# Optimization experiments

Measured on AMD Instinct MI355X. Metric: run time of the kernel, lower is better.

Reference implementation:

```python
import jax, jax.numpy as jnp
import numpy as np

N_SRC = 2_000_000
N_TAR = 2_000_000

def _make_covs(key, n):
    # 3x3 SPD block embedded in a 4x4 (last row/col zero), as in GICP covariances
    A = jax.random.normal(key, (n, 3, 3), dtype=jnp.float32)
    cov3 = 0.1 * jnp.einsum('nij,nkj->nik', A, A) + 0.1 * jnp.eye(3, dtype=jnp.float32)
    covs = jnp.zeros((n, 4, 4), dtype=jnp.float32)
    return covs.at[:, :3, :3].set(cov3)

def setup_inputs() -> dict:
    key = jax.random.key(0)
    k1, k2, k3, k4, k5, k6 = jax.random.split(key, 6)
    # homogeneous points (x, y, z, 1)
    src_xyz = jax.random.normal(k1, (N_SRC, 3), dtype=jnp.float32) * 5.0
    tar_xyz = jax.random.normal(k2, (N_TAR, 3), dtype=jnp.float32) * 5.0
    ones_s = jnp.ones((N_SRC, 1), dtype=jnp.float32)
    ones_t = jnp.ones((N_TAR, 1), dtype=jnp.float32)
    src_points = jnp.concatenate([src_xyz, ones_s], axis=1)
    tar_points = jnp.concatenate([tar_xyz, ones_t], axis=1)
    covs_src = _make_covs(k3, N_SRC)
    covs_tar = _make_covs(k4, N_TAR)
    # transformation: near-identity SE(3)-ish 4x4 (param in the original model)
    transformation = jnp.eye(4, dtype=jnp.float32) + 0.01 * jax.random.normal(k5, (4, 4), dtype=jnp.float32)
    # nearest-neighbor indices (kdtree result in the original, non-differentiable)
    nearest_indices = jax.random.randint(k6, (N_SRC,), 0, N_TAR, dtype=jnp.int64 if jax.config.jax_enable_x64 else jnp.int32)
    return {
        'transformation': transformation,
        'src_points': src_points,
        'tar_points': tar_points,
        'covs_src': covs_src,
        'covs_tar': covs_tar,
        'nearest_indices': nearest_indices,
    }

def reference(transformation, src_points, tar_points, covs_src, covs_tar, nearest_indices):
    # transformed_src_points = src_points @ T  (N,4)
    transformed_src = src_points @ transformation
    # gather KNN-matched target points / covariances
    sel_tar = tar_points[nearest_indices]          # (N,4)
    sel_covs_tar = covs_tar[nearest_indices]       # (N,4,4)
    # T @ C_src @ T^T per point
    tcov = jnp.einsum('ij,njk,lk->nil', transformation, covs_src, transformation)
    RCR = sel_covs_tar + tcov                      # (N,4,4)
    inv_RCR = jnp.linalg.inv(RCR[:, :3, :3])       # (N,3,3)
    res = sel_tar[:, :3] - transformed_src[:, :3]  # (N,3)
    maha = jnp.einsum('ni,nij,nj->n', res, inv_RCR, res)
    return 0.5 * jnp.mean(maha)
```

## Files before the change

### kernel.cpp

```cpp
#include <hip/hip_runtime.h>
#include <stdint.h>

#define BLOCK        256
#define UNROLL       4
#define MAX_BLOCKS   4096

typedef float f32x4 __attribute__((ext_vector_type(4)));

__device__ __forceinline__ float gicp_point(
    int i,
    const float t00, const float t01, const float t02,
    const float t10, const float t11, const float t12,
    const float t20, const float t21, const float t22,
    const float t30, const float t31, const float t32,
    const f32x4* __restrict__ src, const f32x4* __restrict__ tar,
    const f32x4* __restrict__ cs,  const f32x4* __restrict__ ct,
    const int*   __restrict__ idx)
{
    const int   j  = __builtin_nontemporal_load(&idx[i]);
    const f32x4 s  = __builtin_nontemporal_load(&src[i]);
    const f32x4 tp = tar[j];

    const size_t bj = (size_t)j * 4;
    const f32x4 d0 = ct[bj + 0];
    const f32x4 d1 = ct[bj + 1];
    const f32x4 d2 = ct[bj + 2];

    const size_t bi = (size_t)i * 4;
    const f32x4 c0 = __builtin_nontemporal_load(&cs[bi + 0]);
    const f32x4 c1 = __builtin_nontemporal_load(&cs[bi + 1]);
    const f32x4 c2 = __builtin_nontemporal_load(&cs[bi + 2]);

    const float ts0 = s.x * t00 + s.y * t10 + s.z * t20 + s.w * t30;
    const float ts1 = s.x * t01 + s.y * t11 + s.z * t21 + s.w * t31;
    const float ts2 = s.x * t02 + s.y * t12 + s.z * t22 + s.w * t32;
    const float r0 = tp.x - ts0;
    const float r1 = tp.y - ts1;
    const float r2 = tp.z - ts2;

    const float u00 = t00*c0.x + t01*c1.x + t02*c2.x;
    const float u01 = t00*c0.y + t01*c1.y + t02*c2.y;
    const float u02 = t00*c0.z + t01*c1.z + t02*c2.z;
    const float u10 = t10*c0.x + t11*c1.x + t12*c2.x;
    const float u11 = t10*c0.y + t11*c1.y + t12*c2.y;
    const float u12 = t10*c0.z + t11*c1.z + t12*c2.z;
    const float u20 = t20*c0.x + t21*c1.x + t22*c2.x;
    const float u21 = t20*c0.y + t21*c1.y + t22*c2.y;
    const float u22 = t20*c0.z + t21*c1.z + t22*c2.z;

    const float tc00 = u00*t00 + u01*t01 + u02*t02;
    const float tc01 = u00*t10 + u01*t11 + u02*t12;
    const float tc02 = u00*t20 + u01*t21 + u02*t22;
    const float tc11 = u10*t10 + u11*t11 + u12*t12;
    const float tc12 = u10*t20 + u11*t21 + u12*t22;
    const float tc22 = u20*t20 + u21*t21 + u22*t22;

    const float a = d0.x + tc00;
    const float b = d0.y + tc01;
    const float c = d0.z + tc02;
    const float d = d1.y + tc11;
    const float e = d1.z + tc12;
    const float f = d2.z + tc22;

    const float A00 = d * f - e * e;
    const float A01 = c * e - b * f;
    const float A02 = b * e - c * d;
    const float A11 = a * f - c * c;
    const float A12 = b * c - a * e;
    const float A22 = a * d - b * b;

    const float det = a * A00 + b * A01 + c * A02;

    const float num = r0 * r0 * A00 + r1 * r1 * A11 + r2 * r2 * A22
                    + 2.0f * (r0 * r1 * A01 + r0 * r2 * A02 + r1 * r2 * A12);

    return num / det;
}

__global__ __launch_bounds__(BLOCK) void gicp_maha_kernel(
    const float* __restrict__ T,
    const f32x4* __restrict__ src,
    const f32x4* __restrict__ tar,
    const f32x4* __restrict__ cs,
    const f32x4* __restrict__ ct,
    const int*   __restrict__ idx,
    float*       __restrict__ partial,
    int n)
{
    const float t00 = T[0],  t01 = T[1],  t02 = T[2];
    const float t10 = T[4],  t11 = T[5],  t12 = T[6];
    const float t20 = T[8],  t21 = T[9],  t22 = T[10];
    const float t30 = T[12], t31 = T[13], t32 = T[14];

    const int stride = gridDim.x * BLOCK;
    const int step   = stride * UNROLL;

    float local = 0.0f;
    for (int base = blockIdx.x * BLOCK + threadIdx.x; base < n; base += step) {
        if (base + 3 * stride < n) {
            float v0 = gicp_point(base,            t00,t01,t02,t10,t11,t12,t20,t21,t22,t30,t31,t32, src,tar,cs,ct,idx);
            float v1 = gicp_point(base +   stride, t00,t01,t02,t10,t11,t12,t20,t21,t22,t30,t31,t32, src,tar,cs,ct,idx);
            float v2 = gicp_point(base + 2*stride, t00,t01,t02,t10,t11,t12,t20,t21,t22,t30,t31,t32, src,tar,cs,ct,idx);
            float v3 = gicp_point(base + 3*stride, t00,t01,t02,t10,t11,t12,t20,t21,t22,t30,t31,t32, src,tar,cs,ct,idx);
            local += (v0 + v1) + (v2 + v3);
        } else {
            #pragma unroll
            for (int k = 0; k < UNROLL; ++k) {
                int i = base + k * stride;
                const float m = (i < n) ? 1.0f : 0.0f;
                i = (i < n) ? i : (n - 1);
                local += m * gicp_point(i, t00,t01,t02,t10,t11,t12,t20,t21,t22,t30,t31,t32, src,tar,cs,ct,idx);
            }
        }
    }

    for (int off = 32; off > 0; off >>= 1)
        local += __shfl_down(local, off, 64);

    __shared__ float wsum[BLOCK / 64];
    const int wave = threadIdx.x >> 6;
    if ((threadIdx.x & 63) == 0) wsum[wave] = local;
    __syncthreads();
    if (threadIdx.x == 0) {
        float s = wsum[0];
        #pragma unroll
        for (int w = 1; w < BLOCK / 64; ++w) s += wsum[w];
        partial[blockIdx.x] = s;
    }
}

__global__ __launch_bounds__(256) void gicp_finalize_kernel(
    const float* __restrict__ partial, float* __restrict__ out,
    double scale, int nblocks)
{
    double s = 0.0;
    for (int k = threadIdx.x; k < nblocks; k += 256)
        s += (double)partial[k];
    for (int off = 32; off > 0; off >>= 1)
        s += __shfl_down(s, off, 64);
    __shared__ double wsum[4];
    const int wave = threadIdx.x >> 6;
    if ((threadIdx.x & 63) == 0) wsum[wave] = s;
    __syncthreads();
    if (threadIdx.x == 0)
        out[0] = (float)((wsum[0] + wsum[1] + wsum[2] + wsum[3]) * scale);
}

extern "C" void kernel_launch(void* const* d_in, const int* in_sizes, int n_in,
                              void* d_out, int out_size, void* d_ws, size_t ws_size,
                              hipStream_t stream) {
    const float* T   = (const float*)d_in[0];
    const f32x4* src = (const f32x4*)d_in[1];
    const f32x4* tar = (const f32x4*)d_in[2];
    const f32x4* cs  = (const f32x4*)d_in[3];
    const f32x4* ct  = (const f32x4*)d_in[4];
    const int*   idx = (const int*)d_in[5];
    const int n = in_sizes[1] / 4;

    int nblocks = (n + BLOCK * UNROLL - 1) / (BLOCK * UNROLL);
    if (nblocks < 1) nblocks = 1;
    if (nblocks > MAX_BLOCKS) nblocks = MAX_BLOCKS;
    const int ws_cap = (int)(ws_size / sizeof(float));
    if (nblocks > ws_cap) nblocks = ws_cap;

    float* partial = (float*)d_ws;

    gicp_maha_kernel<<<nblocks, BLOCK, 0, stream>>>(T, src, tar, cs, ct, idx,
                                                    partial, n);
    gicp_finalize_kernel<<<1, 256, 0, stream>>>(partial, (float*)d_out,
                                                0.5 / (double)n, nblocks);
}
```

Baseline: 351.6 us.

## Prepack target covariance and point into one 64-byte record for gathers

Adds a pre-pass that interleaves the first three target covariance rows with the target point into one 64-byte record per target. The main kernel's random gather then touches a single cache line per neighbour instead of two separate arrays. When the workspace is too small to hold the records, it instead runs a cache-warming pass that streams the target arrays before the direct kernel. The pre-pass adds a full extra read and write of the target data each call. The record buffer is sized from the source count rather than the target count.

```diff
diff --git a/kernel.cpp b/kernel.cpp
--- a/kernel.cpp
+++ b/kernel.cpp
@@ -1,36 +1,51 @@
 #include <hip/hip_runtime.h>
 #include <stdint.h>
 
-#define BLOCK        256
-#define UNROLL       4
-#define MAX_BLOCKS   4096
+#define BLOCK          256
+#define UNROLL         4
+#define MAX_BLOCKS     4096
+#define PREPACK_BLOCKS 2048
+#define WARM_BLOCKS    2048
 
 typedef float f32x4 __attribute__((ext_vector_type(4)));
 
-__device__ __forceinline__ float gicp_point(
-    int i,
+__global__ __launch_bounds__(256) void prepack_kernel(
+    const f32x4* __restrict__ tar,
+    const f32x4* __restrict__ ct,
+    f32x4*       __restrict__ rec,
+    long n4)
+{
+    const long stride = (long)gridDim.x * 256;
+    for (long k = (long)blockIdx.x * 256 + threadIdx.x; k < n4; k += stride) {
+        f32x4 v;
+        if ((k & 3) == 3) v = __builtin_nontemporal_load(&tar[k >> 2]);
+        else              v = __builtin_nontemporal_load(&ct[k]);
+        rec[k] = v;
+    }
+}
+
+__global__ __launch_bounds__(256) void llc_warm_kernel(
+    const f32x4* __restrict__ tar, long ntar4,
+    const f32x4* __restrict__ ct,  long nct4)
+{
+    const long stride = (long)gridDim.x * 256;
+    f32x4 acc = {0.f, 0.f, 0.f, 0.f};
+    for (long k = (long)blockIdx.x * 256 + threadIdx.x; k < nct4; k += stride)
+        acc += ct[k];
+    for (long k = (long)blockIdx.x * 256 + threadIdx.x; k < ntar4; k += stride)
+        acc += tar[k];
+    asm volatile("" :: "v"(acc.x), "v"(acc.y), "v"(acc.z), "v"(acc.w));
+}
+
+__device__ __forceinline__ float gicp_math(
+    const f32x4 s, const f32x4 tp,
+    const f32x4 c0, const f32x4 c1, const f32x4 c2,
+    const f32x4 d0, const f32x4 d1, const f32x4 d2,
     const float t00, const float t01, const float t02,
     const float t10, const float t11, const float t12,
     const float t20, const float t21, const float t22,
-    const float t30, const float t31, const float t32,
-    const f32x4* __restrict__ src, const f32x4* __restrict__ tar,
-    const f32x4* __restrict__ cs,  const f32x4* __restrict__ ct,
-    const int*   __restrict__ idx)
-{
-    const int   j  = __builtin_nontemporal_load(&idx[i]);
-    const f32x4 s  = __builtin_nontemporal_load(&src[i]);
-    const f32x4 tp = tar[j];
-
-    const size_t bj = (size_t)j * 4;
-    const f32x4 d0 = ct[bj + 0];
-    const f32x4 d1 = ct[bj + 1];
-    const f32x4 d2 = ct[bj + 2];
-
-    const size_t bi = (size_t)i * 4;
-    const f32x4 c0 = __builtin_nontemporal_load(&cs[bi + 0]);
-    const f32x4 c1 = __builtin_nontemporal_load(&cs[bi + 1]);
-    const f32x4 c2 = __builtin_nontemporal_load(&cs[bi + 2]);
-
+    const float t30, const float t31, const float t32)
+{
     const float ts0 = s.x * t00 + s.y * t10 + s.z * t20 + s.w * t30;
     const float ts1 = s.x * t01 + s.y * t11 + s.z * t21 + s.w * t31;
     const float ts2 = s.x * t02 + s.y * t12 + s.z * t22 + s.w * t32;
@@ -70,14 +85,115 @@
     const float A22 = a * d - b * b;
 
     const float det = a * A00 + b * A01 + c * A02;
-
     const float num = r0 * r0 * A00 + r1 * r1 * A11 + r2 * r2 * A22
                     + 2.0f * (r0 * r1 * A01 + r0 * r2 * A02 + r1 * r2 * A12);
-
     return num / det;
 }
 
-__global__ __launch_bounds__(BLOCK) void gicp_maha_kernel(
+__device__ __forceinline__ float gicp_point_rec(
+    int i,
+    const float t00, const float t01, const float t02,
+    const float t10, const float t11, const float t12,
+    const float t20, const float t21, const float t22,
+    const float t30, const float t31, const float t32,
+    const f32x4* __restrict__ src, const f32x4* __restrict__ cs,
+    const f32x4* __restrict__ rec, const int* __restrict__ idx)
+{
+    const int   j  = __builtin_nontemporal_load(&idx[i]);
+    const f32x4 s  = __builtin_nontemporal_load(&src[i]);
+
+    const size_t bj = (size_t)j * 4;
+    const f32x4 d0 = rec[bj + 0];
+    const f32x4 d1 = rec[bj + 1];
+    const f32x4 d2 = rec[bj + 2];
+    const f32x4 tp = rec[bj + 3];
+
+    const size_t bi = (size_t)i * 4;
+    const f32x4 c0 = __builtin_nontemporal_load(&cs[bi + 0]);
+    const f32x4 c1 = __builtin_nontemporal_load(&cs[bi + 1]);
+    const f32x4 c2 = __builtin_nontemporal_load(&cs[bi + 2]);
+
+    return gicp_math(s, tp, c0, c1, c2, d0, d1, d2,
+                     t00,t01,t02,t10,t11,t12,t20,t21,t22,t30,t31,t32);
+}
+
+__device__ __forceinline__ float gicp_point_dir(
+    int i,
+    const float t00, const float t01, const float t02,
+    const float t10, const float t11, const float t12,
+    const float t20, const float t21, const float t22,
+    const float t30, const float t31, const float t32,
+    const f32x4* __restrict__ src, const f32x4* __restrict__ tar,
+    const f32x4* __restrict__ cs,  const f32x4* __restrict__ ct,
+    const int*   __restrict__ idx)
+{
+    const int   j  = __builtin_nontemporal_load(&idx[i]);
+    const f32x4 s  = __builtin_nontemporal_load(&src[i]);
+    const f32x4 tp = tar[j];
+    const size_t bj = (size_t)j * 4;
+    const f32x4 d0 = ct[bj + 0];
+    const f32x4 d1 = ct[bj + 1];
+    const f32x4 d2 = ct[bj + 2];
+    const size_t bi = (size_t)i * 4;
+    const f32x4 c0 = __builtin_nontemporal_load(&cs[bi + 0]);
+    const f32x4 c1 = __builtin_nontemporal_load(&cs[bi + 1]);
+    const f32x4 c2 = __builtin_nontemporal_load(&cs[bi + 2]);
+    return gicp_math(s, tp, c0, c1, c2, d0, d1, d2,
+                     t00,t01,t02,t10,t11,t12,t20,t21,t22,t30,t31,t32);
+}
+
+#define TLOAD  const float t00 = T[0],  t01 = T[1],  t02 = T[2]; \
+               const float t10 = T[4],  t11 = T[5],  t12 = T[6]; \
+               const float t20 = T[8],  t21 = T[9],  t22 = T[10]; \
+               const float t30 = T[12], t31 = T[13], t32 = T[14];
+
+__global__ __launch_bounds__(BLOCK) void gicp_maha_rec_kernel(
+    const float* __restrict__ T,
+    const f32x4* __restrict__ src,
+    const f32x4* __restrict__ cs,
+    const f32x4* __restrict__ rec,
+    const int*   __restrict__ idx,
+    float*       __restrict__ partial,
+    int n)
+{
+    TLOAD
+    const int stride = gridDim.x * BLOCK;
+    const int step   = stride * UNROLL;
+
+    float local = 0.0f;
+    for (int base = blockIdx.x * BLOCK + threadIdx.x; base < n; base += step) {
+        if (base + 3 * stride < n) {
+            float v0 = gicp_point_rec(base,            t00,t01,t02,t10,t11,t12,t20,t21,t22,t30,t31,t32, src,cs,rec,idx);
+            float v1 = gicp_point_rec(base +   stride, t00,t01,t02,t10,t11,t12,t20,t21,t22,t30,t31,t32, src,cs,rec,idx);
+            float v2 = gicp_point_rec(base + 2*stride, t00,t01,t02,t10,t11,t12,t20,t21,t22,t30,t31,t32, src,cs,rec,idx);
+            float v3 = gicp_point_rec(base + 3*stride, t00,t01,t02,t10,t11,t12,t20,t21,t22,t30,t31,t32, src,cs,rec,idx);
+            local += (v0 + v1) + (v2 + v3);
+        } else {
+            #pragma unroll
+            for (int k = 0; k < UNROLL; ++k) {
+                int i = base + k * stride;
+                const float m = (i < n) ? 1.0f : 0.0f;
+                i = (i < n) ? i : (n - 1);
+                local += m * gicp_point_rec(i, t00,t01,t02,t10,t11,t12,t20,t21,t22,t30,t31,t32, src,cs,rec,idx);
+            }
+        }
+    }
+
+    for (int off = 32; off > 0; off >>= 1)
+        local += __shfl_down(local, off, 64);
+    __shared__ float wsum[BLOCK / 64];
+    const int wave = threadIdx.x >> 6;
+    if ((threadIdx.x & 63) == 0) wsum[wave] = local;
+    __syncthreads();
+    if (threadIdx.x == 0) {
+        float s = wsum[0];
+        #pragma unroll
+        for (int w = 1; w < BLOCK / 64; ++w) s += wsum[w];
+        partial[blockIdx.x] = s;
+    }
+}
+
+__global__ __launch_bounds__(BLOCK) void gicp_maha_dir_kernel(
     const float* __restrict__ T,
     const f32x4* __restrict__ src,
     const f32x4* __restrict__ tar,
@@ -87,21 +203,17 @@
     float*       __restrict__ partial,
     int n)
 {
-    const float t00 = T[0],  t01 = T[1],  t02 = T[2];
-    const float t10 = T[4],  t11 = T[5],  t12 = T[6];
-    const float t20 = T[8],  t21 = T[9],  t22 = T[10];
-    const float t30 = T[12], t31 = T[13], t32 = T[14];
-
+    TLOAD
     const int stride = gridDim.x * BLOCK;
     const int step   = stride * UNROLL;
 
     float local = 0.0f;
     for (int base = blockIdx.x * BLOCK + threadIdx.x; base < n; base += step) {
         if (base + 3 * stride < n) {
-            float v0 = gicp_point(base,            t00,t01,t02,t10,t11,t12,t20,t21,t22,t30,t31,t32, src,tar,cs,ct,idx);
-            float v1 = gicp_point(base +   stride, t00,t01,t02,t10,t11,t12,t20,t21,t22,t30,t31,t32, src,tar,cs,ct,idx);
-            float v2 = gicp_point(base + 2*stride, t00,t01,t02,t10,t11,t12,t20,t21,t22,t30,t31,t32, src,tar,cs,ct,idx);
-            float v3 = gicp_point(base + 3*stride, t00,t01,t02,t10,t11,t12,t20,t21,t22,t30,t31,t32, src,tar,cs,ct,idx);
+            float v0 = gicp_point_dir(base,            t00,t01,t02,t10,t11,t12,t20,t21,t22,t30,t31,t32, src,tar,cs,ct,idx);
+            float v1 = gicp_point_dir(base +   stride, t00,t01,t02,t10,t11,t12,t20,t21,t22,t30,t31,t32, src,tar,cs,ct,idx);
+            float v2 = gicp_point_dir(base + 2*stride, t00,t01,t02,t10,t11,t12,t20,t21,t22,t30,t31,t32, src,tar,cs,ct,idx);
+            float v3 = gicp_point_dir(base + 3*stride, t00,t01,t02,t10,t11,t12,t20,t21,t22,t30,t31,t32, src,tar,cs,ct,idx);
             local += (v0 + v1) + (v2 + v3);
         } else {
             #pragma unroll
@@ -109,14 +221,13 @@
                 int i = base + k * stride;
                 const float m = (i < n) ? 1.0f : 0.0f;
                 i = (i < n) ? i : (n - 1);
-                local += m * gicp_point(i, t00,t01,t02,t10,t11,t12,t20,t21,t22,t30,t31,t32, src,tar,cs,ct,idx);
+                local += m * gicp_point_dir(i, t00,t01,t02,t10,t11,t12,t20,t21,t22,t30,t31,t32, src,tar,cs,ct,idx);
             }
         }
     }
 
     for (int off = 32; off > 0; off >>= 1)
         local += __shfl_down(local, off, 64);
-
     __shared__ float wsum[BLOCK / 64];
     const int wave = threadIdx.x >> 6;
     if ((threadIdx.x & 63) == 0) wsum[wave] = local;
@@ -160,13 +271,25 @@
     int nblocks = (n + BLOCK * UNROLL - 1) / (BLOCK * UNROLL);
     if (nblocks < 1) nblocks = 1;
     if (nblocks > MAX_BLOCKS) nblocks = MAX_BLOCKS;
-    const int ws_cap = (int)(ws_size / sizeof(float));
+
+    const size_t rec_off   = 16384;
+    const size_t rec_bytes = (size_t)n * 64;
+    float* partial = (float*)d_ws;
+    const int ws_cap = MAX_BLOCKS;
     if (nblocks > ws_cap) nblocks = ws_cap;
 
-    float* partial = (float*)d_ws;
-
-    gicp_maha_kernel<<<nblocks, BLOCK, 0, stream>>>(T, src, tar, cs, ct, idx,
-                                                    partial, n);
+    if (ws_size >= rec_off + rec_bytes) {
+        f32x4* rec = (f32x4*)((char*)d_ws + rec_off);
+        prepack_kernel<<<PREPACK_BLOCKS, 256, 0, stream>>>(tar, ct, rec,
+                                                           (long)n * 4);
+        gicp_maha_rec_kernel<<<nblocks, BLOCK, 0, stream>>>(T, src, cs, rec,
+                                                            idx, partial, n);
+    } else {
+        llc_warm_kernel<<<WARM_BLOCKS, 256, 0, stream>>>(
+            tar, (long)in_sizes[2] / 4, ct, (long)in_sizes[4] / 4);
+        gicp_maha_dir_kernel<<<nblocks, BLOCK, 0, stream>>>(T, src, tar, cs,
+                                                            ct, idx, partial, n);
+    }
     gicp_finalize_kernel<<<1, 256, 0, stream>>>(partial, (float*)d_out,
                                                 0.5 / (double)n, nblocks);
 }
```

Result: slower. 371.0 us (+5.5%).
